# Kernel tuning notes

Hardware: AMD Instinct MI355X
Metric: run time of the kernel (lower is better)

Reference implementation:

```python
import jax, jax.numpy as jnp
import numpy as np

N_HEAD = 16
N_KV_HEADS = 4
HEAD_SIZE = 128  # n_embd // n_head = 2048 // 16


def setup_inputs() -> dict:
    key = jax.random.key(0)
    k0, k1, k2 = jax.random.split(key, 3)
    B, T, C = 4, 2048, 2048
    kv_dim = N_KV_HEADS * HEAD_SIZE  # 512
    x = jax.random.normal(k0, (B, T, C), dtype=jnp.float32)
    W_attn = jax.random.normal(k1, (C, C + 2 * kv_dim), dtype=jnp.float32) * 0.02
    b_attn = jnp.zeros((C + 2 * kv_dim,), dtype=jnp.float32)
    W_proj = jax.random.normal(k2, (C, C), dtype=jnp.float32) * 0.02
    b_proj = jnp.zeros((C,), dtype=jnp.float32)
    return {"x": x, "W_attn": W_attn, "b_attn": b_attn, "W_proj": W_proj, "b_proj": b_proj}


def reference(x, W_attn, b_attn, W_proj, b_proj):
    B, T, C = x.shape
    hs = HEAD_SIZE
    kv_dim = N_KV_HEADS * hs
    qkv = x @ W_attn + b_attn                      # [B,T,C+2*kv_dim]
    q, k, v = jnp.split(qkv, [C, C + kv_dim], axis=2)
    q = q.reshape(B, T, N_HEAD, hs).transpose(0, 2, 1, 3)       # [B,H,T,hs]
    k = k.reshape(B, T, N_KV_HEADS, hs).transpose(0, 2, 1, 3)   # [B,Hkv,T,hs]
    v = v.reshape(B, T, N_KV_HEADS, hs).transpose(0, 2, 1, 3)
    # GQA: repeat_interleave kv heads to match query heads
    rep = N_HEAD // N_KV_HEADS
    k_r = jnp.repeat(k, rep, axis=1)               # [B,H,T,hs]
    v_r = jnp.repeat(v, rep, axis=1)
    scale = 1.0 / jnp.sqrt(jnp.float32(hs))
    scores = jnp.einsum('bhqd,bhkd->bhqk', q, k_r) * scale      # [B,H,T,T]
    causal = jnp.tril(jnp.ones((T, T), dtype=bool))
    scores = jnp.where(causal, scores, jnp.finfo(scores.dtype).min)
    attn = jax.nn.softmax(scores, axis=-1)
    y = jnp.einsum('bhqk,bhkd->bhqd', attn, v_r)   # [B,H,T,hs]
    y = y.transpose(0, 2, 1, 3).reshape(B, T, C)
    y = y @ W_proj + b_proj
    return y
```

## Files before the change

kernel.cpp:

```cpp
#include <hip/hip_runtime.h>
#include <stdint.h>

#define DEVI __device__ __forceinline__

typedef __attribute__((ext_vector_type(8))) uint16_t u16x8;
typedef __attribute__((ext_vector_type(4))) uint16_t u16x4v;
typedef __attribute__((ext_vector_type(4))) uint32_t u32x4;
typedef __attribute__((ext_vector_type(8))) __bf16 bf16x8;
typedef __attribute__((ext_vector_type(4))) float f32x4;
typedef __attribute__((ext_vector_type(16))) float f32x16;

DEVI uint16_t f2bf(float x) {
  union { float f; uint32_t u; } v; v.f = x;
  return (uint16_t)((v.u + 0x7fffu + ((v.u >> 16) & 1u)) >> 16);
}

DEVI uint16_t f2bfn(float f) {
  __bf16 h = (__bf16)f;
  return __builtin_bit_cast(uint16_t, h);
}

DEVI f32x4 mfma16(u16x8 a, u16x8 b, f32x4 c) {
  return __builtin_amdgcn_mfma_f32_16x16x32_bf16(
      __builtin_bit_cast(bf16x8, a), __builtin_bit_cast(bf16x8, b), c, 0, 0, 0);
}

DEVI f32x16 mfma32(u16x8 a, u16x8 b, f32x16 c) {
  return __builtin_amdgcn_mfma_f32_32x32x16_bf16(
      __builtin_bit_cast(bf16x8, a), __builtin_bit_cast(bf16x8, b), c, 0, 0, 0);
}

DEVI void async16(void* lds, const void* g) {
  __builtin_amdgcn_global_load_lds(
      (const __attribute__((address_space(1))) uint32_t*)g,
      (__attribute__((address_space(3))) uint32_t*)lds, 16, 0, 0);
}

#define QSC 0.12751742925f

__global__ void cvt_f32_bf16(const float* __restrict__ in, uint16_t* __restrict__ out, int n4) {
  int i = blockIdx.x * blockDim.x + threadIdx.x;
  const int st = gridDim.x * blockDim.x;
  for (; i < n4; i += st) {
    float4 v = ((const float4*)in)[i];
    u16x4v o;
    o[0] = f2bf(v.x); o[1] = f2bf(v.y); o[2] = f2bf(v.z); o[3] = f2bf(v.w);
    ((u16x4v*)out)[i] = o;
  }
}

__global__ void transp_cvt(const float* __restrict__ in, uint16_t* __restrict__ out,
                           int K, int N) {
  __shared__ float Ws[64][65];
  const int n0 = blockIdx.x * 64, k0 = blockIdx.y * 64;
  const int t = threadIdx.x;
  const int r = t >> 4, c = (t & 15) << 2;
#pragma unroll
  for (int it = 0; it < 4; ++it) {
    float4 v = *(const float4*)&in[(size_t)(k0 + it * 16 + r) * N + n0 + c];
    Ws[it * 16 + r][c] = v.x; Ws[it * 16 + r][c + 1] = v.y;
    Ws[it * 16 + r][c + 2] = v.z; Ws[it * 16 + r][c + 3] = v.w;
  }
  __syncthreads();
#pragma unroll
  for (int it = 0; it < 4; ++it) {
    const int rr = it * 16 + r;
    const int cc = c;
    ushort4 o;
    o.x = f2bf(Ws[cc][rr]);     o.y = f2bf(Ws[cc + 1][rr]);
    o.z = f2bf(Ws[cc + 2][rr]); o.w = f2bf(Ws[cc + 3][rr]);
    *(ushort4*)&out[(size_t)(n0 + rr) * K + k0 + cc] = o;
  }
}

__global__ void transp_v(const uint16_t* __restrict__ in, uint16_t* __restrict__ out, int T) {
  __shared__ uint16_t Vsm[64][72];
  const int t0 = blockIdx.x * 64, d0 = blockIdx.y * 64, bh = blockIdx.z;
  const uint16_t* ip = in + (size_t)bh * T * 128;
  uint16_t* op = out + (size_t)bh * 128 * T;
  const int t = threadIdx.x;
  const int r = t >> 3, c = (t & 7) << 3;
#pragma unroll
  for (int it = 0; it < 2; ++it) {
    u16x8 v = *(const u16x8*)&ip[(size_t)(t0 + it * 32 + r) * 128 + d0 + c];
#pragma unroll
    for (int j = 0; j < 8; ++j) Vsm[it * 32 + r][c + j] = v[j];
  }
  __syncthreads();
#pragma unroll
  for (int it = 0; it < 2; ++it) {
    const int rr = it * 32 + r;
    const int cc = c;
    u16x8 o;
#pragma unroll
    for (int j = 0; j < 8; ++j) o[j] = Vsm[cc + j][rr];
    *(u16x8*)&op[(size_t)(d0 + rr) * T + t0 + cc] = o;
  }
}

__global__ __launch_bounds__(512, 1)
void gemm_qkv(const uint16_t* __restrict__ A, const uint16_t* __restrict__ Bt,
              const float* __restrict__ bias,
              uint16_t* __restrict__ q, uint16_t* __restrict__ kk, uint16_t* __restrict__ v,
              int M, int N, int K) {
  constexpr int BK = 64;
  __shared__ uint16_t As[2][256 * BK];
  __shared__ uint16_t Bs[2][128 * BK];
  int bid = (int)blockIdx.x;
  const int q8 = (int)gridDim.x >> 3;
  bid = (bid & 7) * q8 + (bid >> 3);
  const int nbn = N >> 7;
  const int brow = (bid / nbn) << 8;
  const int bcol = (bid % nbn) << 7;
  const int t = threadIdx.x;
  const int wid = t >> 6, lane = t & 63;
  const int wm = wid >> 1, wn = wid & 1;
  const int lr = lane & 15, g = lane >> 4, l7 = lr & 7;

  const int logch = (((t & 7) ^ ((t >> 3) & 7)) << 3);
  const uint16_t* Asrc = A + (size_t)(brow + (t >> 3)) * K + logch;
  const uint16_t* Bsrc = Bt + (size_t)(bcol + (t >> 3)) * K + logch;
  const size_t skip64 = (size_t)64 * K;
  const int dt = t * 8;

  auto stageA = [&](int buf, int k0) {
#pragma unroll
    for (int l = 0; l < 4; ++l)
      async16(&As[buf][l * 4096 + dt], Asrc + (size_t)l * skip64 + k0);
  };
  auto stageB = [&](int buf, int k0) {
#pragma unroll
    for (int l = 0; l < 2; ++l)
      async16(&Bs[buf][l * 4096 + dt], Bsrc + (size_t)l * skip64 + k0);
  };

  f32x4 acc[4][4];
#pragma unroll
  for (int i = 0; i < 4; ++i)
#pragma unroll
    for (int j = 0; j < 4; ++j) acc[i][j] = f32x4{0.f, 0.f, 0.f, 0.f};

  const int nt = K / BK;
  stageA(0, 0); stageB(0, 0);
  if (nt > 1) stageB(1, BK);
  asm volatile("s_waitcnt vmcnt(0)" ::: "memory");
  __builtin_amdgcn_s_barrier();

  for (int tt = 0; tt < nt; ++tt) {
    const int buf = tt & 1;
    u16x8 bfr[4][2];
#pragma unroll
    for (int p = 0; p < 2; ++p) {
      if (p == 0) {
#pragma unroll
        for (int j = 0; j < 4; ++j) {
          const int brw = wn * 64 + j * 16 + lr;
#pragma unroll
          for (int s = 0; s < 2; ++s)
            bfr[j][s] = *(const u16x8*)&Bs[buf][brw * 64 + ((((s << 2) + g) ^ l7) << 3)];
        }
      }
      u16x8 af[2][2];
#pragma unroll
      for (int ii = 0; ii < 2; ++ii) {
        const int arow = wm * 64 + (p * 2 + ii) * 16 + lr;
#pragma unroll
        for (int s = 0; s < 2; ++s)
          af[ii][s] = *(const u16x8*)&As[buf][arow * 64 + ((((s << 2) + g) ^ l7) << 3)];
      }
      if (p == 0) {
        if (tt + 1 < nt) stageA(buf ^ 1, (tt + 1) * BK);
      } else {
        if (tt + 2 < nt) {
          stageB(buf, (tt + 2) * BK);
          asm volatile("s_waitcnt vmcnt(2)" ::: "memory");
        } else {
          asm volatile("s_waitcnt vmcnt(0)" ::: "memory");
        }
      }
      __builtin_amdgcn_s_barrier();
      __builtin_amdgcn_s_setprio(1);
#pragma unroll
      for (int ii = 0; ii < 2; ++ii)
#pragma unroll
        for (int j = 0; j < 4; ++j)
#pragma unroll
          for (int s = 0; s < 2; ++s)
            acc[p * 2 + ii][j] = mfma16(af[ii][s], bfr[j][s], acc[p * 2 + ii][j]);
      __builtin_amdgcn_s_setprio(0);
      __builtin_amdgcn_s_barrier();
    }
  }

#pragma unroll
  for (int i = 0; i < 4; ++i) {
#pragma unroll
    for (int j = 0; j < 4; ++j) {
      const int col = bcol + wn * 64 + j * 16 + lr;
      const float bb = bias[col];
#pragma unroll
      for (int r = 0; r < 4; ++r) {
        const int row = brow + wm * 64 + i * 16 + (g << 2) + r;
        const float val = acc[i][j][r] + bb;
        const int b_ = row >> 11, tt2 = row & 2047;
        const int d = col & 127;
        if (col < 2048) {
          const int hh = col >> 7;
          q[((size_t)((b_ * 16 + hh) * 2048 + tt2) << 7) + d] = f2bf(val * QSC);
        } else if (col < 2560) {
          const int hh = (col - 2048) >> 7;
          kk[((size_t)((b_ * 4 + hh) * 2048 + tt2) << 7) + d] = f2bf(val);
        } else {
          const int hh = (col - 2560) >> 7;
          v[((size_t)((b_ * 4 + hh) * 2048 + tt2) << 7) + d] = f2bf(val);
        }
      }
    }
  }
}

__global__ __launch_bounds__(512, 1)
void gemm_proj(const uint16_t* __restrict__ A, const uint16_t* __restrict__ Bt,
               const float* __restrict__ bias, float* __restrict__ outF,
               int M, int N, int K) {
  constexpr int BK = 64;
  __shared__ uint16_t As[2][256 * BK];
  __shared__ uint16_t Bs[2][256 * BK];
  int bid = (int)blockIdx.x;
  const int q8 = (int)gridDim.x >> 3;
  bid = (bid & 7) * q8 + (bid >> 3);
  const int nbn = N >> 8;
  const int brow = (bid / nbn) << 8;
  const int bcol = (bid % nbn) << 8;
  const int t = threadIdx.x;
  const int wid = t >> 6, lane = t & 63;
  const int wm = wid >> 2, wn = wid & 3;
  const int lr = lane & 15, g = lane >> 4;
  const int l7 = lr & 7;

  const int sr0 = t >> 3;
  const int logch = (((t & 7) ^ ((t >> 3) & 7)) << 3);
  const uint16_t* Asrc0 = A + (size_t)(brow + sr0) * K + logch;
  const uint16_t* Asrc1 = A + (size_t)(brow + 64 + sr0) * K + logch;
  const uint16_t* Bsrc0 = Bt + (size_t)(bcol + sr0) * K + logch;
  const uint16_t* Bsrc1 = Bt + (size_t)(bcol + 64 + sr0) * K + logch;
  const size_t hskip = (size_t)128 * K;
  const int d0 = t * 8, d1 = 4096 + t * 8;

  auto stageA = [&](int buf, int h, int k0) {
    async16(&As[buf][h * 8192 + d0], Asrc0 + (size_t)h * hskip + k0);
    async16(&As[buf][h * 8192 + d1], Asrc1 + (size_t)h * hskip + k0);
  };
  auto stageB = [&](int buf, int h, int k0) {
    async16(&Bs[buf][h * 8192 + d0], Bsrc0 + (size_t)h * hskip + k0);
    async16(&Bs[buf][h * 8192 + d1], Bsrc1 + (size_t)h * hskip + k0);
  };

  f32x4 acc[8][4];
#pragma unroll
  for (int i = 0; i < 8; ++i)
#pragma unroll
    for (int j = 0; j < 4; ++j) acc[i][j] = f32x4{0.f, 0.f, 0.f, 0.f};

  const int nt = K / BK;
  stageA(0, 0, 0); stageA(0, 1, 0);
  stageB(0, 0, 0); stageB(0, 1, 0);
  if (nt > 1) { stageB(1, 0, BK); stageB(1, 1, BK); }
  asm volatile("s_waitcnt vmcnt(0)" ::: "memory");
  __builtin_amdgcn_s_barrier();

  for (int tt = 0; tt < nt; ++tt) {
    const int buf = tt & 1;
    u16x8 bfr[4][2];
#pragma unroll
    for (int p = 0; p < 4; ++p) {
      if (p == 0) {
#pragma unroll
        for (int j = 0; j < 4; ++j) {
          const int brw = wn * 64 + j * 16 + lr;
#pragma unroll
          for (int s = 0; s < 2; ++s)
            bfr[j][s] = *(const u16x8*)&Bs[buf][brw * 64 + ((((s << 2) + g) ^ l7) << 3)];
        }
      }
      u16x8 af[2][2];
#pragma unroll
      for (int ii = 0; ii < 2; ++ii) {
        const int arow = wm * 128 + (p * 2 + ii) * 16 + lr;
#pragma unroll
        for (int s = 0; s < 2; ++s)
          af[ii][s] = *(const u16x8*)&As[buf][arow * 64 + ((((s << 2) + g) ^ l7) << 3)];
      }
      if (p == 0) { if (tt + 1 < nt) stageA(buf ^ 1, 0, (tt + 1) * BK); }
      if (p == 1) { if (tt + 1 < nt) stageA(buf ^ 1, 1, (tt + 1) * BK); }
      if (p == 2) { if (tt + 2 < nt) stageB(buf, 0, (tt + 2) * BK); }
      if (p == 3) {
        if (tt + 2 < nt) {
          stageB(buf, 1, (tt + 2) * BK);
          asm volatile("s_waitcnt vmcnt(4)" ::: "memory");
        } else {
          asm volatile("s_waitcnt vmcnt(0)" ::: "memory");
        }
      }
      __builtin_amdgcn_s_barrier();
      __builtin_amdgcn_s_setprio(1);
#pragma unroll
      for (int ii = 0; ii < 2; ++ii)
#pragma unroll
        for (int j = 0; j < 4; ++j)
#pragma unroll
          for (int s = 0; s < 2; ++s)
            acc[p * 2 + ii][j] = mfma16(af[ii][s], bfr[j][s], acc[p * 2 + ii][j]);
      __builtin_amdgcn_s_setprio(0);
      __builtin_amdgcn_s_barrier();
    }
  }

#pragma unroll
  for (int i = 0; i < 8; ++i) {
#pragma unroll
    for (int j = 0; j < 4; ++j) {
      const int col = bcol + wn * 64 + j * 16 + lr;
      const float bb = bias[col];
#pragma unroll
      for (int r = 0; r < 4; ++r) {
        const int row = brow + wm * 128 + i * 16 + (g << 2) + r;
        outF[(size_t)row * N + col] = acc[i][j][r] + bb;
      }
    }
  }
}

__global__ __launch_bounds__(512, 1)
void attn_fwd(const uint16_t* __restrict__ Q,
              const uint16_t* __restrict__ Kg,
              const uint16_t* __restrict__ Vt,
              uint16_t* __restrict__ Y,
              int T) {
  __shared__ __align__(16) uint16_t Ks[2][64 * 128];
  __shared__ __align__(16) uint16_t Vs[128 * 64];
  const int id = (int)blockIdx.x;
  const int x = id & 7;
  const int h = (id >> 3) & 15, b = (id >> 7) & 3;
  const int qb = (id & 256) ? 7 - x : x;
  const int hkv = h >> 2;

  const int t = threadIdx.x, w = t >> 6, lane = t & 63;
  const int ql = lane & 31, b5 = lane >> 5;
  const int swzK = (ql & 15) << 3;
  const int swzV = (ql & 7) << 3;

  const uint16_t* Qp = Q + ((size_t)(b * 16 + h) * T + qb * 256) * 128;
  const uint16_t* Kp = Kg + (size_t)(b * 4 + hkv) * T * 128;
  const uint16_t* Vp = Vt + (size_t)(b * 4 + hkv) * 128 * T;

  auto stageK = [&](int buf, int kv0) {
#pragma unroll
    for (int l = 0; l < 2; ++l) {
      const int s = l * 512 + t;
      const int row = s >> 4;
      const int cl = (s & 15) ^ (row & 15);
      async16(&Ks[buf][s * 8], &Kp[(size_t)(kv0 + row) * 128 + cl * 8]);
    }
  };
  auto stageV = [&](int kv0) {
#pragma unroll
    for (int l = 0; l < 2; ++l) {
      const int s = l * 512 + t;
      const int row = s >> 3;
      const int cl = (s & 7) ^ (row & 7);
      async16(&Vs[s * 8], &Vp[(size_t)row * T + kv0 + cl * 8]);
    }
  };

  const int row0 = qb * 256 + w * 32;
  const int qrow = row0 + ql;

  u16x8 qf[8];
#pragma unroll
  for (int kc = 0; kc < 8; ++kc)
    qf[kc] = *(const u16x8*)&Qp[(size_t)(w * 32 + ql) * 128 + kc * 16 + b5 * 8];

  f32x16 o[4];
#pragma unroll
  for (int db = 0; db < 4; ++db)
#pragma unroll
    for (int r = 0; r < 16; ++r) o[db][r] = 0.f;
  float mrow = -3e38f, lrow = 0.f;

  const int ntiles = 4 * qb + 4;
  const int myn = 4 * qb + (w >> 1) + 1;

  stageK(0, 0);
  __syncthreads();

  int cur = 0;
  for (int tile = 0; tile < ntiles; ++tile) {
    const int kv0 = tile << 6;
    stageV(kv0);
    if (tile + 1 < ntiles) stageK(cur ^ 1, (tile + 1) << 6);

    const bool run = tile < myn;
    f32x16 s[2];
    u16x8 pa[4];
    if (run) {
#pragma unroll
      for (int m = 0; m < 2; ++m)
#pragma unroll
        for (int r = 0; r < 16; ++r) s[m][r] = 0.f;
      __builtin_amdgcn_s_setprio(1);
#pragma unroll
      for (int kc = 0; kc < 8; ++kc) {
        const int cc = (kc * 16 + b5 * 8) ^ swzK;
        u16x8 k0f = *(const u16x8*)&Ks[cur][ql * 128 + cc];
        u16x8 k1f = *(const u16x8*)&Ks[cur][(32 + ql) * 128 + cc];
        s[0] = mfma32(k0f, qf[kc], s[0]);
        s[1] = mfma32(k1f, qf[kc], s[1]);
      }
      __builtin_amdgcn_s_setprio(0);

      if (kv0 + 63 > row0) {
#pragma unroll
        for (int m = 0; m < 2; ++m)
#pragma unroll
          for (int r = 0; r < 16; ++r) {
            const int kg = kv0 + 32 * m + (r & 3) + 8 * (r >> 2) + 4 * b5;
            if (kg > qrow) s[m][r] = -3e38f;
          }
      }
      float mt[16];
#pragma unroll
      for (int r = 0; r < 16; ++r) mt[r] = fmaxf(s[0][r], s[1][r]);
#pragma unroll
      for (int st = 8; st >= 1; st >>= 1)
#pragma unroll
        for (int r = 0; r < st; ++r) mt[r] = fmaxf(mt[r], mt[r + st]);
      float mx = fmaxf(mt[0], __shfl_xor(mt[0], 32));
      const bool defer = __all(mx <= mrow + 8.f);
      const float mnew = defer ? mrow : fmaxf(mrow, mx);
      const float sc = defer ? 1.f : exp2f(mrow - mnew);
#pragma unroll
      for (int m = 0; m < 2; ++m)
#pragma unroll
        for (int r = 0; r < 16; ++r) s[m][r] = exp2f(s[m][r] - mnew);
      float pt[16];
#pragma unroll
      for (int r = 0; r < 16; ++r) pt[r] = s[0][r] + s[1][r];
#pragma unroll
      for (int st = 8; st >= 1; st >>= 1)
#pragma unroll
        for (int r = 0; r < st; ++r) pt[r] += pt[r + st];
      float ps = pt[0] + __shfl_xor(pt[0], 32);
      mrow = mnew;
      lrow = lrow * sc + ps;
      if (!defer) {
#pragma unroll
        for (int db = 0; db < 4; ++db)
#pragma unroll
          for (int r = 0; r < 16; ++r) o[db][r] *= sc;
      }

#pragma unroll
      for (int m = 0; m < 2; ++m) {
        uint32_t pw[4][2];
#pragma unroll
        for (int a = 0; a < 4; ++a)
#pragma unroll
          for (int hh = 0; hh < 2; ++hh)
            pw[a][hh] = (uint32_t)f2bfn(s[m][4 * a + 2 * hh]) |
                        ((uint32_t)f2bfn(s[m][4 * a + 2 * hh + 1]) << 16);
#pragma unroll
        for (int c = 0; c < 2; ++c) {
          uint32_t wd[4];
#pragma unroll
          for (int hh = 0; hh < 2; ++hh) {
            const uint32_t mine  = b5 ? pw[2 * c + 1][hh] : pw[2 * c][hh];
            const uint32_t yours = b5 ? pw[2 * c][hh] : pw[2 * c + 1][hh];
            const uint32_t xw = (uint32_t)__shfl_xor((int)yours, 32);
            wd[hh] = b5 ? xw : mine;
            wd[2 + hh] = b5 ? mine : xw;
          }
          u32x4 tmp = {wd[0], wd[1], wd[2], wd[3]};
          pa[2 * m + c] = __builtin_bit_cast(u16x8, tmp);
        }
      }
    }
    __syncthreads();

    if (run) {
      __builtin_amdgcn_s_setprio(1);
#pragma unroll
      for (int db = 0; db < 4; ++db) {
#pragma unroll
        for (int kf = 0; kf < 4; ++kf) {
          u16x8 vf = *(const u16x8*)&Vs[(32 * db + ql) * 64 +
                                        ((kf * 16 + b5 * 8) ^ swzV)];
          o[db] = mfma32(vf, pa[kf], o[db]);
        }
      }
      __builtin_amdgcn_s_setprio(0);
    }
    __syncthreads();
    cur ^= 1;
  }

  uint16_t* Yp = Y + ((size_t)(b * T + row0 + ql)) * 2048 + h * 128 + b5 * 4;
  const float inv = 1.f / lrow;
#pragma unroll
  for (int db = 0; db < 4; ++db)
#pragma unroll
    for (int a = 0; a < 4; ++a) {
      u16x4v pk;
#pragma unroll
      for (int r = 0; r < 4; ++r) pk[r] = f2bfn(o[db][4 * a + r] * inv);
      *(u16x4v*)&Yp[db * 32 + a * 8] = pk;
    }
}

extern "C" void kernel_launch(void* const* d_in, const int* in_sizes, int n_in,
                              void* d_out, int out_size, void* d_ws, size_t ws_size,
                              hipStream_t stream) {
  const float* x      = (const float*)d_in[0];
  const float* W_attn = (const float*)d_in[1];
  const float* b_attn = (const float*)d_in[2];
  const float* W_proj = (const float*)d_in[3];
  const float* b_proj = (const float*)d_in[4];
  float* out = (float*)d_out;

  const int B = 4, T = 2048, C = 2048, H = 16, HKV = 4, HS = 128;
  const int M = B * T;
  const int Nqkv = C + 2 * HKV * HS;

  uint8_t* ws = (uint8_t*)d_ws;
  size_t off = 0;
  auto alloc = [&](size_t bytes) {
    void* p = ws + off;
    off += (bytes + 255) & ~(size_t)255;
    return p;
  };
  uint16_t* xb  = (uint16_t*)alloc((size_t)M * C * 2);
  uint16_t* WaT = (uint16_t*)alloc((size_t)Nqkv * C * 2);
  uint16_t* WpT = (uint16_t*)alloc((size_t)C * C * 2);
  uint16_t* qb  = (uint16_t*)alloc((size_t)B * H * T * HS * 2);
  uint16_t* kb  = (uint16_t*)alloc((size_t)B * HKV * T * HS * 2);
  uint16_t* vb  = (uint16_t*)alloc((size_t)B * HKV * T * HS * 2);
  uint16_t* vtb = (uint16_t*)alloc((size_t)B * HKV * HS * T * 2);
  uint16_t* yb  = xb;

  cvt_f32_bf16<<<2048, 256, 0, stream>>>(x, xb, M * C / 4);
  transp_cvt<<<dim3(Nqkv / 64, C / 64), 256, 0, stream>>>(W_attn, WaT, C, Nqkv);
  transp_cvt<<<dim3(C / 64, C / 64), 256, 0, stream>>>(W_proj, WpT, C, C);
  gemm_qkv<<<dim3((M / 256) * (Nqkv / 128)), 512, 0, stream>>>(
      xb, WaT, b_attn, qb, kb, vb, M, Nqkv, C);
  transp_v<<<dim3(T / 64, 2, B * HKV), 256, 0, stream>>>(vb, vtb, T);
  attn_fwd<<<dim3(512), 512, 0, stream>>>(qb, kb, vtb, yb, T);
  gemm_proj<<<dim3((M / 256) * (C / 256)), 512, 0, stream>>>(
      yb, WpT, b_proj, out, M, C, C);
}
```

Before: 345.4 us.

## Fuse V transpose into QKV epilogue and shrink attention blocks to 128 rows

The QKV GEMM epilogue now writes V directly in transposed [b,hkv,d,t] layout as packed 4-element stores, which removes the separate transp_v kernel and its intermediate buffer. The attention kernel is restructured to 256-thread blocks with 128 query rows, 32-key tiles, smaller shared memory and a 4-blocks-per-CU launch bound, using a lookup table to balance causal work across 1024 blocks. This aims for better occupancy and load balance, at the cost of more barriers per key and less K/V reuse per tile.

```diff
diff --git a/kernel.cpp b/kernel.cpp
--- a/kernel.cpp
+++ b/kernel.cpp
@@ -73,35 +73,10 @@
   }
 }
 
-__global__ void transp_v(const uint16_t* __restrict__ in, uint16_t* __restrict__ out, int T) {
-  __shared__ uint16_t Vsm[64][72];
-  const int t0 = blockIdx.x * 64, d0 = blockIdx.y * 64, bh = blockIdx.z;
-  const uint16_t* ip = in + (size_t)bh * T * 128;
-  uint16_t* op = out + (size_t)bh * 128 * T;
-  const int t = threadIdx.x;
-  const int r = t >> 3, c = (t & 7) << 3;
-#pragma unroll
-  for (int it = 0; it < 2; ++it) {
-    u16x8 v = *(const u16x8*)&ip[(size_t)(t0 + it * 32 + r) * 128 + d0 + c];
-#pragma unroll
-    for (int j = 0; j < 8; ++j) Vsm[it * 32 + r][c + j] = v[j];
-  }
-  __syncthreads();
-#pragma unroll
-  for (int it = 0; it < 2; ++it) {
-    const int rr = it * 32 + r;
-    const int cc = c;
-    u16x8 o;
-#pragma unroll
-    for (int j = 0; j < 8; ++j) o[j] = Vsm[cc + j][rr];
-    *(u16x8*)&op[(size_t)(d0 + rr) * T + t0 + cc] = o;
-  }
-}
-
 __global__ __launch_bounds__(512, 1)
 void gemm_qkv(const uint16_t* __restrict__ A, const uint16_t* __restrict__ Bt,
               const float* __restrict__ bias,
-              uint16_t* __restrict__ q, uint16_t* __restrict__ kk, uint16_t* __restrict__ v,
+              uint16_t* __restrict__ q, uint16_t* __restrict__ kk, uint16_t* __restrict__ vt,
               int M, int N, int K) {
   constexpr int BK = 64;
   __shared__ uint16_t As[2][256 * BK];
@@ -198,22 +173,28 @@
     for (int j = 0; j < 4; ++j) {
       const int col = bcol + wn * 64 + j * 16 + lr;
       const float bb = bias[col];
-#pragma unroll
-      for (int r = 0; r < 4; ++r) {
-        const int row = brow + wm * 64 + i * 16 + (g << 2) + r;
-        const float val = acc[i][j][r] + bb;
-        const int b_ = row >> 11, tt2 = row & 2047;
-        const int d = col & 127;
-        if (col < 2048) {
-          const int hh = col >> 7;
-          q[((size_t)((b_ * 16 + hh) * 2048 + tt2) << 7) + d] = f2bf(val * QSC);
-        } else if (col < 2560) {
-          const int hh = (col - 2048) >> 7;
-          kk[((size_t)((b_ * 4 + hh) * 2048 + tt2) << 7) + d] = f2bf(val);
-        } else {
-          const int hh = (col - 2560) >> 7;
-          v[((size_t)((b_ * 4 + hh) * 2048 + tt2) << 7) + d] = f2bf(val);
-        }
+      const int rowb = brow + wm * 64 + i * 16 + (g << 2);
+      const int b_ = rowb >> 11, ttb = rowb & 2047;
+      const int d = col & 127;
+      float vals[4];
+#pragma unroll
+      for (int r = 0; r < 4; ++r) vals[r] = acc[i][j][r] + bb;
+      if (col < 2048) {
+        const int hh = col >> 7;
+#pragma unroll
+        for (int r = 0; r < 4; ++r)
+          q[((size_t)((b_ * 16 + hh) * 2048 + ttb + r) << 7) + d] = f2bf(vals[r] * QSC);
+      } else if (col < 2560) {
+        const int hh = (col - 2048) >> 7;
+#pragma unroll
+        for (int r = 0; r < 4; ++r)
+          kk[((size_t)((b_ * 4 + hh) * 2048 + ttb + r) << 7) + d] = f2bf(vals[r]);
+      } else {
+        const int hh = (col - 2560) >> 7;
+        u16x4v pk;
+#pragma unroll
+        for (int r = 0; r < 4; ++r) pk[r] = f2bf(vals[r]);
+        *(u16x4v*)&vt[(((size_t)((b_ * 4 + hh) * 128 + d)) << 11) + ttb] = pk;
       }
     }
   }
@@ -331,33 +312,34 @@
   }
 }
 
-__global__ __launch_bounds__(512, 1)
+__global__ __launch_bounds__(256, 4)
 void attn_fwd(const uint16_t* __restrict__ Q,
               const uint16_t* __restrict__ Kg,
               const uint16_t* __restrict__ Vt,
               uint16_t* __restrict__ Y,
               int T) {
-  __shared__ __align__(16) uint16_t Ks[2][64 * 128];
-  __shared__ __align__(16) uint16_t Vs[128 * 64];
+  __shared__ __align__(16) uint16_t Ks[2][32 * 128];
+  __shared__ __align__(16) uint16_t Vs[128 * 32];
+  const int QTAB[16] = {0,2,4,6, 15,13,11,9, 1,3,5,7, 14,12,10,8};
   const int id = (int)blockIdx.x;
-  const int x = id & 7;
-  const int h = (id >> 3) & 15, b = (id >> 7) & 3;
-  const int qb = (id & 256) ? 7 - x : x;
+  const int bh = id & 63;
+  const int b = bh >> 4, h = bh & 15;
+  const int qb = QTAB[id >> 6];
   const int hkv = h >> 2;
 
   const int t = threadIdx.x, w = t >> 6, lane = t & 63;
   const int ql = lane & 31, b5 = lane >> 5;
   const int swzK = (ql & 15) << 3;
-  const int swzV = (ql & 7) << 3;
-
-  const uint16_t* Qp = Q + ((size_t)(b * 16 + h) * T + qb * 256) * 128;
+  const int swzV = (((ql & 3) ^ ((ql >> 2) & 3))) << 3;
+
+  const uint16_t* Qp = Q + ((size_t)(b * 16 + h) * T + qb * 128) * 128;
   const uint16_t* Kp = Kg + (size_t)(b * 4 + hkv) * T * 128;
   const uint16_t* Vp = Vt + (size_t)(b * 4 + hkv) * 128 * T;
 
   auto stageK = [&](int buf, int kv0) {
 #pragma unroll
     for (int l = 0; l < 2; ++l) {
-      const int s = l * 512 + t;
+      const int s = l * 256 + t;
       const int row = s >> 4;
       const int cl = (s & 15) ^ (row & 15);
       async16(&Ks[buf][s * 8], &Kp[(size_t)(kv0 + row) * 128 + cl * 8]);
@@ -366,14 +348,14 @@
   auto stageV = [&](int kv0) {
 #pragma unroll
     for (int l = 0; l < 2; ++l) {
-      const int s = l * 512 + t;
-      const int row = s >> 3;
-      const int cl = (s & 7) ^ (row & 7);
+      const int s = l * 256 + t;
+      const int row = s >> 2;
+      const int cl = (s & 3) ^ ((row & 3) ^ ((row >> 2) & 3));
       async16(&Vs[s * 8], &Vp[(size_t)row * T + kv0 + cl * 8]);
     }
   };
 
-  const int row0 = qb * 256 + w * 32;
+  const int row0 = qb * 128 + w * 32;
   const int qrow = row0 + ql;
 
   u16x8 qf[8];
@@ -389,50 +371,44 @@
   float mrow = -3e38f, lrow = 0.f;
 
   const int ntiles = 4 * qb + 4;
-  const int myn = 4 * qb + (w >> 1) + 1;
+  const int myn = 4 * qb + w + 1;
 
   stageK(0, 0);
   __syncthreads();
 
   int cur = 0;
   for (int tile = 0; tile < ntiles; ++tile) {
-    const int kv0 = tile << 6;
+    const int kv0 = tile << 5;
     stageV(kv0);
-    if (tile + 1 < ntiles) stageK(cur ^ 1, (tile + 1) << 6);
+    if (tile + 1 < ntiles) stageK(cur ^ 1, (tile + 1) << 5);
 
     const bool run = tile < myn;
-    f32x16 s[2];
-    u16x8 pa[4];
+    f32x16 s;
+    u16x8 pa[2];
     if (run) {
 #pragma unroll
-      for (int m = 0; m < 2; ++m)
-#pragma unroll
-        for (int r = 0; r < 16; ++r) s[m][r] = 0.f;
+      for (int r = 0; r < 16; ++r) s[r] = 0.f;
       __builtin_amdgcn_s_setprio(1);
 #pragma unroll
       for (int kc = 0; kc < 8; ++kc) {
         const int cc = (kc * 16 + b5 * 8) ^ swzK;
-        u16x8 k0f = *(const u16x8*)&Ks[cur][ql * 128 + cc];
-        u16x8 k1f = *(const u16x8*)&Ks[cur][(32 + ql) * 128 + cc];
-        s[0] = mfma32(k0f, qf[kc], s[0]);
-        s[1] = mfma32(k1f, qf[kc], s[1]);
+        u16x8 kf = *(const u16x8*)&Ks[cur][ql * 128 + cc];
+        s = mfma32(kf, qf[kc], s);
       }
       __builtin_amdgcn_s_setprio(0);
 
-      if (kv0 + 63 > row0) {
-#pragma unroll
-        for (int m = 0; m < 2; ++m)
-#pragma unroll
-          for (int r = 0; r < 16; ++r) {
-            const int kg = kv0 + 32 * m + (r & 3) + 8 * (r >> 2) + 4 * b5;
-            if (kg > qrow) s[m][r] = -3e38f;
-          }
-      }
-      float mt[16];
-#pragma unroll
-      for (int r = 0; r < 16; ++r) mt[r] = fmaxf(s[0][r], s[1][r]);
-#pragma unroll
-      for (int st = 8; st >= 1; st >>= 1)
+      if (kv0 + 31 > row0) {
+#pragma unroll
+        for (int r = 0; r < 16; ++r) {
+          const int kg = kv0 + (r & 3) + 8 * (r >> 2) + 4 * b5;
+          if (kg > qrow) s[r] = -3e38f;
+        }
+      }
+      float mt[8];
+#pragma unroll
+      for (int r = 0; r < 8; ++r) mt[r] = fmaxf(s[r], s[r + 8]);
+#pragma unroll
+      for (int st = 4; st >= 1; st >>= 1)
 #pragma unroll
         for (int r = 0; r < st; ++r) mt[r] = fmaxf(mt[r], mt[r + st]);
       float mx = fmaxf(mt[0], __shfl_xor(mt[0], 32));
@@ -440,14 +416,12 @@
       const float mnew = defer ? mrow : fmaxf(mrow, mx);
       const float sc = defer ? 1.f : exp2f(mrow - mnew);
 #pragma unroll
-      for (int m = 0; m < 2; ++m)
-#pragma unroll
-        for (int r = 0; r < 16; ++r) s[m][r] = exp2f(s[m][r] - mnew);
-      float pt[16];
-#pragma unroll
-      for (int r = 0; r < 16; ++r) pt[r] = s[0][r] + s[1][r];
-#pragma unroll
-      for (int st = 8; st >= 1; st >>= 1)
+      for (int r = 0; r < 16; ++r) s[r] = exp2f(s[r] - mnew);
+      float pt[8];
+#pragma unroll
+      for (int r = 0; r < 8; ++r) pt[r] = s[r] + s[r + 8];
+#pragma unroll
+      for (int st = 4; st >= 1; st >>= 1)
 #pragma unroll
         for (int r = 0; r < st; ++r) pt[r] += pt[r + st];
       float ps = pt[0] + __shfl_xor(pt[0], 32);
@@ -460,29 +434,26 @@
           for (int r = 0; r < 16; ++r) o[db][r] *= sc;
       }
 
-#pragma unroll
-      for (int m = 0; m < 2; ++m) {
-        uint32_t pw[4][2];
-#pragma unroll
-        for (int a = 0; a < 4; ++a)
-#pragma unroll
-          for (int hh = 0; hh < 2; ++hh)
-            pw[a][hh] = (uint32_t)f2bfn(s[m][4 * a + 2 * hh]) |
-                        ((uint32_t)f2bfn(s[m][4 * a + 2 * hh + 1]) << 16);
-#pragma unroll
-        for (int c = 0; c < 2; ++c) {
-          uint32_t wd[4];
-#pragma unroll
-          for (int hh = 0; hh < 2; ++hh) {
-            const uint32_t mine  = b5 ? pw[2 * c + 1][hh] : pw[2 * c][hh];
-            const uint32_t yours = b5 ? pw[2 * c][hh] : pw[2 * c + 1][hh];
-            const uint32_t xw = (uint32_t)__shfl_xor((int)yours, 32);
-            wd[hh] = b5 ? xw : mine;
-            wd[2 + hh] = b5 ? mine : xw;
-          }
-          u32x4 tmp = {wd[0], wd[1], wd[2], wd[3]};
-          pa[2 * m + c] = __builtin_bit_cast(u16x8, tmp);
-        }
+      uint32_t pw[4][2];
+#pragma unroll
+      for (int a = 0; a < 4; ++a)
+#pragma unroll
+        for (int hh = 0; hh < 2; ++hh)
+          pw[a][hh] = (uint32_t)f2bfn(s[4 * a + 2 * hh]) |
+                      ((uint32_t)f2bfn(s[4 * a + 2 * hh + 1]) << 16);
+#pragma unroll
+      for (int c = 0; c < 2; ++c) {
+        uint32_t wd[4];
+#pragma unroll
+        for (int hh = 0; hh < 2; ++hh) {
+          const uint32_t mine  = b5 ? pw[2 * c + 1][hh] : pw[2 * c][hh];
+          const uint32_t yours = b5 ? pw[2 * c][hh] : pw[2 * c + 1][hh];
+          const uint32_t xw = (uint32_t)__shfl_xor((int)yours, 32);
+          wd[hh] = b5 ? xw : mine;
+          wd[2 + hh] = b5 ? mine : xw;
+        }
+        u32x4 tmp = {wd[0], wd[1], wd[2], wd[3]};
+        pa[c] = __builtin_bit_cast(u16x8, tmp);
       }
     }
     __syncthreads();
@@ -492,8 +463,8 @@
 #pragma unroll
       for (int db = 0; db < 4; ++db) {
 #pragma unroll
-        for (int kf = 0; kf < 4; ++kf) {
-          u16x8 vf = *(const u16x8*)&Vs[(32 * db + ql) * 64 +
+        for (int kf = 0; kf < 2; ++kf) {
+          u16x8 vf = *(const u16x8*)&Vs[(32 * db + ql) * 32 +
                                         ((kf * 16 + b5 * 8) ^ swzV)];
           o[db] = mfma32(vf, pa[kf], o[db]);
         }
@@ -543,7 +514,6 @@
   uint16_t* WpT = (uint16_t*)alloc((size_t)C * C * 2);
   uint16_t* qb  = (uint16_t*)alloc((size_t)B * H * T * HS * 2);
   uint16_t* kb  = (uint16_t*)alloc((size_t)B * HKV * T * HS * 2);
-  uint16_t* vb  = (uint16_t*)alloc((size_t)B * HKV * T * HS * 2);
   uint16_t* vtb = (uint16_t*)alloc((size_t)B * HKV * HS * T * 2);
   uint16_t* yb  = xb;
 
@@ -551,9 +521,8 @@
   transp_cvt<<<dim3(Nqkv / 64, C / 64), 256, 0, stream>>>(W_attn, WaT, C, Nqkv);
   transp_cvt<<<dim3(C / 64, C / 64), 256, 0, stream>>>(W_proj, WpT, C, C);
   gemm_qkv<<<dim3((M / 256) * (Nqkv / 128)), 512, 0, stream>>>(
-      xb, WaT, b_attn, qb, kb, vb, M, Nqkv, C);
-  transp_v<<<dim3(T / 64, 2, B * HKV), 256, 0, stream>>>(vb, vtb, T);
-  attn_fwd<<<dim3(512), 512, 0, stream>>>(qb, kb, vtb, yb, T);
+      xb, WaT, b_attn, qb, kb, vtb, M, Nqkv, C);
+  attn_fwd<<<dim3(1024), 256, 0, stream>>>(qb, kb, vtb, yb, T);
   gemm_proj<<<dim3((M / 256) * (C / 256)), 512, 0, stream>>>(
       yb, WpT, b_proj, out, M, C, C);
 }
```

Result: slower. 429.7 us (+24.4%).
